# Optimization experiments

Hardware: AMD Instinct MI355X
Metric: run time of the kernel (lower is better)

The kernel has to match this reference:

```python
import jax, jax.numpy as jnp
import numpy as np
from jax import lax

NUM_CLASSES = 10
NUM_ITER = 3
CAP_DIM = 8       # primary capsule dim
OUT_CAP_DIM = 16  # digit capsule dim
NUM_MAP = 32      # 256 / 8
NUM_PRIM = 144    # 12*12


def squash(x, axis=-1):
    s2 = jnp.sum(x * x, axis=axis, keepdims=True)
    return (s2 / (1.0 + s2)) * x / jnp.sqrt(s2 + 1e-8)


def conv2d(x, w, b):
    y = lax.conv_general_dilated(x, w, (1, 1), 'VALID',
                                 dimension_numbers=('NCHW', 'OIHW', 'NCHW'))
    return y + b[None, :, None, None]


def setup_inputs() -> dict:
    key = jax.random.key(0)
    ks = jax.random.split(key, 13)
    B = 128
    return {
        'imgs': jax.random.uniform(ks[0], (B, 1, 28, 28), dtype=jnp.float32),
        'conv1_w': jax.random.normal(ks[1], (256, 1, 9, 9), jnp.float32) * 0.05,
        'conv1_b': jnp.zeros((256,), jnp.float32),
        'conv2_w': jax.random.normal(ks[2], (256, 256, 9, 9), jnp.float32) * 0.02,
        'conv2_b': jnp.zeros((256,), jnp.float32),
        # non-shared routing weights: [num_prim_map, num_prim_cap, num_classes, out_dim, in_dim]
        'W_digit': jax.random.normal(ks[3], (NUM_MAP, NUM_PRIM, NUM_CLASSES, OUT_CAP_DIM, CAP_DIM), jnp.float32),
        'dec_w1': jax.random.normal(ks[4], (OUT_CAP_DIM * NUM_CLASSES, 512), jnp.float32) * 0.05,
        'dec_b1': jnp.zeros((512,), jnp.float32),
        'dec_w2': jax.random.normal(ks[5], (512, 1024), jnp.float32) * 0.04,
        'dec_b2': jnp.zeros((1024,), jnp.float32),
        'dec_w3': jax.random.normal(ks[6], (1024, 784), jnp.float32) * 0.03,
        'dec_b3': jnp.zeros((784,), jnp.float32),
    }


def capsnet_fwd(imgs, conv1_w, conv1_b, conv2_w, conv2_b, W_digit,
                dec_w1, dec_b1, dec_w2, dec_b2, dec_w3, dec_b3):
    B = imgs.shape[0]
    # conv1 + relu: [B,256,20,20]
    x = jax.nn.relu(conv2d(imgs, conv1_w, conv1_b))
    # primary caps conv: [B,256,12,12]
    p = conv2d(x, conv2_w, conv2_b)
    # view [B, cap_dim, num_map, 12, 12] -> [B, num_map, 144, cap_dim]
    p = p.reshape(B, CAP_DIM, NUM_MAP, NUM_PRIM)
    p = jnp.transpose(p, (0, 2, 3, 1))
    u = squash(p, axis=-1)  # [B, 32, 144, 8]

    # u_hat[b,m,p,c,o] = W[m,p,c,o,i] * u[b,m,p,i]  (broadcast instead of repeat)
    u_hat = jnp.einsum('mpcoi,bmpi->bmpco', W_digit, u)
    u_hat = u_hat.reshape(B, NUM_MAP * NUM_PRIM, NUM_CLASSES, OUT_CAP_DIM)  # [B,4608,10,16]

    # dynamic routing
    b_ij = jnp.zeros((B, NUM_MAP * NUM_PRIM, NUM_CLASSES), u_hat.dtype)
    v = None
    for i in range(NUM_ITER):
        c_ij = jax.nn.softmax(b_ij, axis=1)                     # over input capsules
        s_j = jnp.einsum('bnc,bncd->bcd', c_ij, u_hat)          # [B,10,16]
        v = squash(s_j, axis=-1)
        if i != NUM_ITER - 1:
            b_ij = b_ij + jnp.einsum('bncd,bcd->bnc', u_hat, v)  # agreement

    # v: [B,10,16]
    v_length = jnp.sqrt(jnp.sum(v * v, axis=-1))                 # [B,10]
    y_pred = jnp.argmax(v_length, axis=1)
    y_pred_ohe = jax.nn.one_hot(y_pred, NUM_CLASSES, dtype=jnp.int32)

    masked = (v * y_pred_ohe.astype(v.dtype)[:, :, None]).reshape(B, -1)  # [B,160]
    h = jax.nn.relu(masked @ dec_w1 + dec_b1)
    h = jax.nn.relu(h @ dec_w2 + dec_b2)
    img_reconst = jax.nn.sigmoid(h @ dec_w3 + dec_b3)            # [B,784]
    return y_pred_ohe, img_reconst, v_length


def reference(imgs, conv1_w, conv1_b, conv2_w, conv2_b, W_digit,
              dec_w1, dec_b1, dec_w2, dec_b2, dec_w3, dec_b3):
    return capsnet_fwd(imgs, conv1_w, conv1_b, conv2_w, conv2_b, W_digit,
                       dec_w1, dec_b1, dec_w2, dec_b2, dec_w3, dec_b3)
```

## Files before the change

### kernel.cpp

```cpp
#include <hip/hip_runtime.h>
#include <cstdint>
#include <cstddef>

#define BB 128
#define NMAP 32
#define NPRIM 144
#define NCAP 4608
#define NCLS 10
#define ODIM 16
#define IDIM 8

#define WS_X1H  0
#define WS_X1L  6553600
#define WS_BH   13107200
#define WS_BL   15761408
#define WS_P    18415616
#define WS_U    23134208
#define WS_V    27852800
#define WS_H1   27873280
#define WS_H2   27938816
#define WS_CLS  28069888

#define OUT_REC  1280
#define OUT_LEN  101632

typedef __attribute__((ext_vector_type(8))) short short8;
typedef __attribute__((ext_vector_type(4))) float f32x4;

static __device__ __forceinline__ ushort f2bf(float f) {
    uint u = __float_as_uint(f);
    u = (u + 0x7FFFu + ((u >> 16) & 1u)) >> 16;
    return (ushort)u;
}
static __device__ __forceinline__ float bf2f(ushort h) {
    return __uint_as_float(((uint)h) << 16);
}


__global__ __launch_bounds__(256) void k_conv1(const float* __restrict__ img,
                                               const float* __restrict__ w,
                                               const float* __restrict__ bias,
                                               ushort* __restrict__ x1h,
                                               ushort* __restrict__ x1l) {
    __shared__ float simg[252];
    int bi = blockIdx.x;
    int y = bi % 20;
    int b = bi / 20;
    int oc = threadIdx.x;
    if (threadIdx.x < 252)
        simg[threadIdx.x] = img[(size_t)b * 784 + y * 28 + threadIdx.x];
    __syncthreads();

    float acc[20];
    float bv = bias[oc];
#pragma unroll
    for (int x = 0; x < 20; ++x) acc[x] = bv;
    const float* wp = w + oc * 81;
#pragma unroll
    for (int kh = 0; kh < 9; ++kh) {
        float r[28];
#pragma unroll
        for (int j = 0; j < 28; ++j) r[j] = simg[kh * 28 + j];
#pragma unroll
        for (int kw = 0; kw < 9; ++kw) {
            float wv = wp[kh * 9 + kw];
#pragma unroll
            for (int x = 0; x < 20; ++x)
                acc[x] = fmaf(wv, r[x + kw], acc[x]);
        }
    }
    size_t base = ((size_t)b * 400 + y * 20) * 256 + oc;
#pragma unroll
    for (int x = 0; x < 20; ++x) {
        float v = fmaxf(acc[x], 0.f);
        ushort h = f2bf(v);
        ushort lo = f2bf(v - bf2f(h));
        x1h[base + (size_t)x * 256] = h;
        x1l[base + (size_t)x * 256] = lo;
    }
}

__global__ __launch_bounds__(256) void k_prep_w(const float* __restrict__ w2,
                                                ushort* __restrict__ bh,
                                                ushort* __restrict__ bl) {
    int id = blockIdx.x * 256 + threadIdx.x;
    const float* src = w2 + (size_t)id * 81;
#pragma unroll 9
    for (int t = 0; t < 81; ++t) {
        float v = src[t];
        ushort h = f2bf(v);
        ushort lo = f2bf(v - bf2f(h));
        bh[(size_t)t * 65536 + id] = h;
        bl[(size_t)t * 65536 + id] = lo;
    }
}

static __device__ __forceinline__ f32x4 mfma16(short8 a, short8 b, f32x4 c) {
    return __builtin_amdgcn_mfma_f32_16x16x32_bf16(a, b, c, 0, 0, 0);
}

template<int NMF>
static __device__ __forceinline__ void tap_loop(
    f32x4 (&acc)[5][2], const ushort* A_lds, const int* celloff,
    const ushort* __restrict__ wbh, const ushort* __restrict__ wbl,
    int boff0, int boff1, int bicc) {
    short8 ah[2][5], al[2][5], bhr[2][2], blr[2][2];
#pragma unroll
    for (int i = 0; i < NMF; ++i) {
        ah[0][i] = *(const short8*)(A_lds + celloff[i]);
        al[0][i] = *(const short8*)(A_lds + 16000 + celloff[i]);
    }
    bhr[0][0] = *(const short8*)(wbh + bicc + boff0);
    bhr[0][1] = *(const short8*)(wbh + bicc + boff1);
    blr[0][0] = *(const short8*)(wbl + bicc + boff0);
    blr[0][1] = *(const short8*)(wbl + bicc + boff1);

#pragma unroll 2
    for (int t = 0; t < 81; ++t) {
        const int cur = t & 1, nxt = cur ^ 1;
        if (t < 80) {
            int tn = t + 1;
            int kh = tn / 9, kw = tn - kh * 9;
            int tapoff = (kh * 20 + kw) * 40;
            size_t bko = (size_t)tn * 65536 + bicc;
            bhr[nxt][0] = *(const short8*)(wbh + bko + boff0);
            bhr[nxt][1] = *(const short8*)(wbh + bko + boff1);
            blr[nxt][0] = *(const short8*)(wbl + bko + boff0);
            blr[nxt][1] = *(const short8*)(wbl + bko + boff1);
#pragma unroll
            for (int i = 0; i < NMF; ++i) {
                ah[nxt][i] = *(const short8*)(A_lds + tapoff + celloff[i]);
                al[nxt][i] = *(const short8*)(A_lds + 16000 + tapoff + celloff[i]);
            }
        }
#pragma unroll
        for (int i = 0; i < NMF; ++i)
#pragma unroll
            for (int j = 0; j < 2; ++j)
                acc[i][j] = mfma16(ah[cur][i], bhr[cur][j], acc[i][j]);
#pragma unroll
        for (int i = 0; i < NMF; ++i)
#pragma unroll
            for (int j = 0; j < 2; ++j)
                acc[i][j] = mfma16(ah[cur][i], blr[cur][j], acc[i][j]);
#pragma unroll
        for (int i = 0; i < NMF; ++i)
#pragma unroll
            for (int j = 0; j < 2; ++j)
                acc[i][j] = mfma16(al[cur][i], bhr[cur][j], acc[i][j]);
    }
}

template<int MF0, int NMF>
static __device__ __forceinline__ void conv2s_epi(
    const f32x4 (&acc)[5][2], const float* __restrict__ bias,
    float* __restrict__ p, int b, int oc0, int nq, int r, int kq) {
#pragma unroll
    for (int j = 0; j < 2; ++j) {
        int oc = oc0 + (nq * 2 + j) * 16 + r;
        float bv = bias[oc];
#pragma unroll
        for (int i = 0; i < NMF; ++i) {
            int row = b * 144 + (MF0 + i) * 16 + kq * 4;
#pragma unroll
            for (int reg = 0; reg < 4; ++reg)
                p[(size_t)(row + reg) * 256 + oc] = acc[i][j][reg] + bv;
        }
    }
}

__global__ __launch_bounds__(512, 2) void k_conv2s(
    const ushort* __restrict__ x1h, const ushort* __restrict__ x1l,
    const ushort* __restrict__ wbh, const ushort* __restrict__ wbl,
    const float* __restrict__ bias, float* __restrict__ p) {
    __shared__ ushort A_lds[32000];

    const int tid = threadIdx.x;
    const int lane = tid & 63;
    const int wv = tid >> 6;
    const int mh = wv >> 2;
    const int nq = wv & 3;
    const int b  = blockIdx.x >> 1;
    const int nt = blockIdx.x & 1;
    const int oc0 = nt * 128;
    const int r = lane & 15, kq = lane >> 4;
    const int MF0r = mh ? 5 : 0;

    int celloff[5];
#pragma unroll
    for (int i = 0; i < 5; ++i) {
        int lm = (MF0r + i) * 16 + r;
        celloff[i] = ((lm / 12) * 20 + (lm % 12)) * 40 + kq * 8;
    }
    const int boff0 = (oc0 + (nq * 2 + 0) * 16 + r) * 256 + kq * 8;
    const int boff1 = (oc0 + (nq * 2 + 1) * 16 + r) * 256 + kq * 8;

    f32x4 acc[5][2];
#pragma unroll
    for (int i = 0; i < 5; ++i)
#pragma unroll
        for (int j = 0; j < 2; ++j)
            acc[i][j] = (f32x4){0.f, 0.f, 0.f, 0.f};

    for (int icc = 0; icc < 8; ++icc) {
        if (icc) __syncthreads();
#pragma unroll
        for (int rd = 0; rd < 7; ++rd) {
            int idx = rd * 512 + tid;
            if (idx < 3200) {
                int comp = (idx >= 1600) ? 1 : 0;
                int ci = idx - comp * 1600;
                int cell = ci >> 2, cc = ci & 3;
                const ushort* src = (comp ? x1l : x1h) +
                    ((size_t)b * 400 + cell) * 256 + icc * 32 + cc * 8;
                short8 val = *(const short8*)src;
                *(short8*)(A_lds + comp * 16000 + cell * 40 + cc * 8) = val;
            }
        }
        __syncthreads();
        int bicc = icc * 32;
        if (mh == 0) tap_loop<5>(acc, A_lds, celloff, wbh, wbl, boff0, boff1, bicc);
        else         tap_loop<4>(acc, A_lds, celloff, wbh, wbl, boff0, boff1, bicc);
    }

    if (mh == 0) conv2s_epi<0, 5>(acc, bias, p, b, oc0, nq, r, kq);
    else         conv2s_epi<5, 4>(acc, bias, p, b, oc0, nq, r, kq);
}

__global__ __launch_bounds__(256) void k_squash(const float* __restrict__ p,
                                                float* __restrict__ u) {
    int id = blockIdx.x * 256 + threadIdx.x;
    int n = id % NCAP;
    int b = id / NCAP;
    int m = n / NPRIM, pos = n - m * NPRIM;
    const float* pp = p + ((size_t)b * 144 + pos) * 256 + m;
    float pv[8];
    float s2 = 0.f;
#pragma unroll
    for (int i = 0; i < 8; ++i) {
        pv[i] = pp[i * 32];
        s2 = fmaf(pv[i], pv[i], s2);
    }
    float f = (s2 / (1.f + s2)) / sqrtf(s2 + 1e-8f);
    float4 a = make_float4(f * pv[0], f * pv[1], f * pv[2], f * pv[3]);
    float4 c = make_float4(f * pv[4], f * pv[5], f * pv[6], f * pv[7]);
    float4* up = (float4*)(u + (size_t)id * 8);
    up[0] = a;
    up[1] = c;
}

__global__ __launch_bounds__(256) void k_prep_wt(const float* __restrict__ Wd,
                                                 float* __restrict__ Wt) {
    __shared__ float S[64][129];
    int c = blockIdx.x % NCLS;
    int nt = blockIdx.x / NCLS;
    int n0 = nt * 64;
    int tid = threadIdx.x;
#pragma unroll
    for (int rep = 0; rep < 32; ++rep) {
        int idx = rep * 256 + tid;
        int nl = idx >> 7, oi = idx & 127;
        S[nl][oi] = Wd[(size_t)(n0 + nl) * 1280 + c * 128 + oi];
    }
    __syncthreads();
#pragma unroll
    for (int rep = 0; rep < 32; ++rep) {
        int idx = rep * 256 + tid;
        int oi = idx >> 6, nl = idx & 63;
        Wt[((size_t)c * 128 + oi) * NCAP + n0 + nl] = S[nl][oi];
    }
}

__global__ __launch_bounds__(256) void k_route5(const float* __restrict__ u,
                                                const float* __restrict__ Wt,
                                                float* __restrict__ v_out) {
    __shared__ float part[4][2][17];
    __shared__ float sums[2][17];
    __shared__ float vsh[2][16];
    int c = blockIdx.x % NCLS;
    int bg = blockIdx.x / NCLS;
    int b0 = bg * 2;
    int tid = threadIdx.x;
    int lane = tid & 63, wvi = tid >> 6;
    const float* WtC = Wt + (size_t)c * 128 * NCAP;

    float bij[18][2];
#pragma unroll
    for (int j = 0; j < 18; ++j) { bij[j][0] = 0.f; bij[j][1] = 0.f; }

    for (int iter = 0; iter < 3; ++iter) {
        float sZ[2] = {0.f, 0.f};
        float sS[2][16];
#pragma unroll
        for (int o = 0; o < 16; ++o) { sS[0][o] = 0.f; sS[1][o] = 0.f; }

        for (int j = 0; j < 18; ++j) {
            int n = j * 256 + tid;
            const float4* up0 = (const float4*)(u + ((size_t)b0 * NCAP + n) * 8);
            const float4* up1 = (const float4*)(u + ((size_t)(b0 + 1) * NCAP + n) * 8);
            float4 a0 = up0[0], a1 = up0[1];
            float4 c0 = up1[0], c1 = up1[1];
            float u0[8] = {a0.x, a0.y, a0.z, a0.w, a1.x, a1.y, a1.z, a1.w};
            float u1[8] = {c0.x, c0.y, c0.z, c0.w, c1.x, c1.y, c1.z, c1.w};
            float uh[2][16];
#pragma unroll
            for (int o = 0; o < 16; ++o) {
                float s0 = 0.f, s1 = 0.f;
#pragma unroll
                for (int i = 0; i < 8; ++i) {
                    float w = WtC[(size_t)(o * 8 + i) * NCAP + n];
                    s0 = fmaf(w, u0[i], s0);
                    s1 = fmaf(w, u1[i], s1);
                }
                uh[0][o] = s0;
                uh[1][o] = s1;
            }
#pragma unroll
            for (int bb = 0; bb < 2; ++bb) {
                float e;
                if (iter == 0) {
                    e = 1.f;
                } else {
                    float agr = 0.f;
#pragma unroll
                    for (int o = 0; o < 16; ++o) agr = fmaf(uh[bb][o], vsh[bb][o], agr);
                    bij[j][bb] += agr;
                    e = __expf(bij[j][bb]);
                }
                sZ[bb] += e;
#pragma unroll
                for (int o = 0; o < 16; ++o) sS[bb][o] = fmaf(e, uh[bb][o], sS[bb][o]);
            }
        }

#pragma unroll
        for (int bb = 0; bb < 2; ++bb) {
            float z = sZ[bb];
#pragma unroll
            for (int d = 32; d >= 1; d >>= 1) z += __shfl_xor(z, d, 64);
            if (lane == 0) part[wvi][bb][0] = z;
#pragma unroll
            for (int o = 0; o < 16; ++o) {
                float s = sS[bb][o];
#pragma unroll
                for (int d = 32; d >= 1; d >>= 1) s += __shfl_xor(s, d, 64);
                if (lane == 0) part[wvi][bb][1 + o] = s;
            }
        }
        __syncthreads();
        if (tid < 34) {
            int bb = tid / 17, k = tid % 17;
            float s = 0.f;
#pragma unroll
            for (int w4 = 0; w4 < 4; ++w4) s += part[w4][bb][k];
            sums[bb][k] = s;
        }
        __syncthreads();
        if (tid < 2) {
            float Z = sums[tid][0];
            float s[16];
            float s2 = 0.f;
#pragma unroll
            for (int o = 0; o < 16; ++o) {
                s[o] = sums[tid][1 + o] / Z;
                s2 = fmaf(s[o], s[o], s2);
            }
            float f = (s2 / (1.f + s2)) / sqrtf(s2 + 1e-8f);
#pragma unroll
            for (int o = 0; o < 16; ++o) vsh[tid][o] = f * s[o];
        }
        __syncthreads();
    }
    if (tid < 32) {
        int bb = tid >> 4, o = tid & 15;
        v_out[((size_t)(b0 + bb) * NCLS + c) * 16 + o] = vsh[bb][o];
    }
}

__global__ __launch_bounds__(64) void k_head(const float* __restrict__ v,
                                             float* __restrict__ out,
                                             int* __restrict__ cls_ws) {
    __shared__ float len2[NCLS];
    __shared__ int cls_sh;
    int b = blockIdx.x, tid = threadIdx.x;
    if (tid < NCLS) {
        float s2 = 0.f;
#pragma unroll
        for (int o = 0; o < 16; ++o) {
            float t = v[((size_t)b * NCLS + tid) * 16 + o];
            s2 = fmaf(t, t, s2);
        }
        len2[tid] = s2;
        out[OUT_LEN + b * NCLS + tid] = sqrtf(s2);
    }
    __syncthreads();
    if (tid == 0) {
        int best = 0;
        float bv = len2[0];
        for (int c2 = 1; c2 < NCLS; ++c2)
            if (len2[c2] > bv) { bv = len2[c2]; best = c2; }
        cls_sh = best;
        cls_ws[b] = best;
    }
    __syncthreads();
    if (tid < NCLS) out[b * NCLS + tid] = (tid == cls_sh) ? 1.0f : 0.0f;
}

__global__ __launch_bounds__(256) void k_dec1(const float* __restrict__ v,
                                              const int* __restrict__ cls_ws,
                                              const float* __restrict__ w1,
                                              const float* __restrict__ b1,
                                              float* __restrict__ h1) {
    int id = blockIdx.x * 256 + threadIdx.x;
    int j = id % 512, b = id / 512;
    int cls = cls_ws[b];
    const float* vp = v + ((size_t)b * NCLS + cls) * 16;
    float acc = b1[j];
#pragma unroll
    for (int o = 0; o < 16; ++o)
        acc = fmaf(vp[o], w1[(size_t)(cls * 16 + o) * 512 + j], acc);
    h1[id] = fmaxf(acc, 0.f);
}

__global__ __launch_bounds__(256) void k_dec2(const float* __restrict__ h1,
                                              const float* __restrict__ w2,
                                              const float* __restrict__ b2,
                                              float* __restrict__ h2) {
    __shared__ float hs[512];
    int bi = blockIdx.x;
    int jc = bi % 4;
    int b = bi / 4;
    int tid = threadIdx.x;
    hs[tid] = h1[b * 512 + tid];
    hs[tid + 256] = h1[b * 512 + tid + 256];
    __syncthreads();
    int j = jc * 256 + tid;
    float acc = b2[j];
#pragma unroll 8
    for (int k = 0; k < 512; ++k)
        acc = fmaf(hs[k], w2[(size_t)k * 1024 + j], acc);
    h2[b * 1024 + j] = fmaxf(acc, 0.f);
}

__global__ __launch_bounds__(256) void k_dec3(const float* __restrict__ h2,
                                              const float* __restrict__ w3,
                                              const float* __restrict__ b3,
                                              float* __restrict__ out) {
    __shared__ float hs[1024];
    int bi = blockIdx.x;
    int jc = bi % 4;
    int b = bi / 4;
    int tid = threadIdx.x;
#pragma unroll
    for (int t = 0; t < 4; ++t) hs[tid + t * 256] = h2[b * 1024 + tid + t * 256];
    __syncthreads();
    int j = jc * 256 + tid;
    if (j < 784) {
        float acc = b3[j];
#pragma unroll 8
        for (int k = 0; k < 1024; ++k)
            acc = fmaf(hs[k], w3[(size_t)k * 784 + j], acc);
        out[OUT_REC + b * 784 + j] = 1.f / (1.f + __expf(-acc));
    }
}

extern "C" void kernel_launch(void* const* d_in, const int* in_sizes, int n_in,
                              void* d_out, int out_size, void* d_ws, size_t ws_size,
                              hipStream_t stream) {
    const float* imgs = (const float*)d_in[0];
    const float* c1w  = (const float*)d_in[1];
    const float* c1b  = (const float*)d_in[2];
    const float* c2w  = (const float*)d_in[3];
    const float* c2b  = (const float*)d_in[4];
    const float* Wd   = (const float*)d_in[5];
    const float* dw1  = (const float*)d_in[6];
    const float* db1  = (const float*)d_in[7];
    const float* dw2  = (const float*)d_in[8];
    const float* db2  = (const float*)d_in[9];
    const float* dw3  = (const float*)d_in[10];
    const float* db3  = (const float*)d_in[11];

    float* out = (float*)d_out;
    float* ws  = (float*)d_ws;
    ushort* x1h = (ushort*)(ws + WS_X1H);
    ushort* x1l = (ushort*)(ws + WS_X1L);
    ushort* wbh = (ushort*)(ws + WS_BH);
    ushort* wbl = (ushort*)(ws + WS_BL);
    float* p    = ws + WS_P;
    float* u    = ws + WS_U;
    float* v    = ws + WS_V;
    float* h1   = ws + WS_H1;
    float* h2   = ws + WS_H2;
    int*   cls  = (int*)(ws + WS_CLS);
    float* wt32 = ws + WS_X1H;

    k_conv1<<<BB * 20, 256, 0, stream>>>(imgs, c1w, c1b, x1h, x1l);
    k_prep_w<<<256, 256, 0, stream>>>(c2w, wbh, wbl);
    k_conv2s<<<BB * 2, 512, 0, stream>>>(x1h, x1l, wbh, wbl, c2b, p);
    k_squash<<<BB * NCAP / 256, 256, 0, stream>>>(p, u);
    k_prep_wt<<<720, 256, 0, stream>>>(Wd, wt32);
    k_route5<<<(BB / 2) * NCLS, 256, 0, stream>>>(u, wt32, v);
    k_head<<<BB, 64, 0, stream>>>(v, out, cls);
    k_dec1<<<BB * 512 / 256, 256, 0, stream>>>(v, cls, dw1, db1, h1);
    k_dec2<<<BB * 4, 256, 0, stream>>>(h1, dw2, db2, h2);
    k_dec3<<<BB * 4, 256, 0, stream>>>(h2, dw3, db3, out);
}
```

Baseline: 1.304 ms.

## Retile conv2 MFMA waves to 3x4 fragments with ping-pong fragment buffers

Changes the per-wave tile in the primary-caps conv from 5x2 to 3x4 MFMA fragments, splitting M across four wave groups and N across two. The tap loop becomes an explicit two-buffer ping-pong with separate load and compute helpers. This raises MFMA count per loaded fragment and reduces LDS reads of A. The costs are more global weight fragment loads per wave and an imbalanced split in which the first wave group does 3 M tiles while the others do 2.

New measurement: 1.851 ms. +42.0%, slower.

```diff
diff --git a/kernel.cpp b/kernel.cpp
--- a/kernel.cpp
+++ b/kernel.cpp
@@ -99,69 +99,78 @@
     return __builtin_amdgcn_mfma_f32_16x16x32_bf16(a, b, c, 0, 0, 0);
 }
 
+
+template<int NMF>
+static __device__ __forceinline__ void load_frags(
+    short8 (&ah)[3], short8 (&al)[3], short8 (&bh)[4], short8 (&bl)[4],
+    const ushort* A_lds, const int* celloff,
+    const ushort* __restrict__ wbh, const ushort* __restrict__ wbl,
+    const int* boff, int tn, int bicc) {
+    int kh = tn / 9, kw = tn - kh * 9;
+    int tapoff = (kh * 20 + kw) * 40;
+    size_t bko = (size_t)tn * 65536 + bicc;
+#pragma unroll
+    for (int i = 0; i < NMF; ++i) {
+        ah[i] = *(const short8*)(A_lds + tapoff + celloff[i]);
+        al[i] = *(const short8*)(A_lds + 16000 + tapoff + celloff[i]);
+    }
+#pragma unroll
+    for (int j = 0; j < 4; ++j) {
+        bh[j] = *(const short8*)(wbh + bko + boff[j]);
+        bl[j] = *(const short8*)(wbl + bko + boff[j]);
+    }
+}
+
+template<int NMF>
+static __device__ __forceinline__ void compute_frags(
+    f32x4 (&acc)[3][4], const short8 (&ah)[3], const short8 (&al)[3],
+    const short8 (&bh)[4], const short8 (&bl)[4]) {
+#pragma unroll
+    for (int i = 0; i < NMF; ++i)
+#pragma unroll
+        for (int j = 0; j < 4; ++j)
+            acc[i][j] = mfma16(ah[i], bh[j], acc[i][j]);
+#pragma unroll
+    for (int i = 0; i < NMF; ++i)
+#pragma unroll
+        for (int j = 0; j < 4; ++j)
+            acc[i][j] = mfma16(ah[i], bl[j], acc[i][j]);
+#pragma unroll
+    for (int i = 0; i < NMF; ++i)
+#pragma unroll
+        for (int j = 0; j < 4; ++j)
+            acc[i][j] = mfma16(al[i], bh[j], acc[i][j]);
+}
+
 template<int NMF>
 static __device__ __forceinline__ void tap_loop(
-    f32x4 (&acc)[5][2], const ushort* A_lds, const int* celloff,
+    f32x4 (&acc)[3][4], const ushort* A_lds, const int* celloff,
     const ushort* __restrict__ wbh, const ushort* __restrict__ wbl,
-    int boff0, int boff1, int bicc) {
-    short8 ah[2][5], al[2][5], bhr[2][2], blr[2][2];
-#pragma unroll
-    for (int i = 0; i < NMF; ++i) {
-        ah[0][i] = *(const short8*)(A_lds + celloff[i]);
-        al[0][i] = *(const short8*)(A_lds + 16000 + celloff[i]);
-    }
-    bhr[0][0] = *(const short8*)(wbh + bicc + boff0);
-    bhr[0][1] = *(const short8*)(wbh + bicc + boff1);
-    blr[0][0] = *(const short8*)(wbl + bicc + boff0);
-    blr[0][1] = *(const short8*)(wbl + bicc + boff1);
-
-#pragma unroll 2
-    for (int t = 0; t < 81; ++t) {
-        const int cur = t & 1, nxt = cur ^ 1;
-        if (t < 80) {
-            int tn = t + 1;
-            int kh = tn / 9, kw = tn - kh * 9;
-            int tapoff = (kh * 20 + kw) * 40;
-            size_t bko = (size_t)tn * 65536 + bicc;
-            bhr[nxt][0] = *(const short8*)(wbh + bko + boff0);
-            bhr[nxt][1] = *(const short8*)(wbh + bko + boff1);
-            blr[nxt][0] = *(const short8*)(wbl + bko + boff0);
-            blr[nxt][1] = *(const short8*)(wbl + bko + boff1);
-#pragma unroll
-            for (int i = 0; i < NMF; ++i) {
-                ah[nxt][i] = *(const short8*)(A_lds + tapoff + celloff[i]);
-                al[nxt][i] = *(const short8*)(A_lds + 16000 + tapoff + celloff[i]);
-            }
-        }
-#pragma unroll
-        for (int i = 0; i < NMF; ++i)
-#pragma unroll
-            for (int j = 0; j < 2; ++j)
-                acc[i][j] = mfma16(ah[cur][i], bhr[cur][j], acc[i][j]);
-#pragma unroll
-        for (int i = 0; i < NMF; ++i)
-#pragma unroll
-            for (int j = 0; j < 2; ++j)
-                acc[i][j] = mfma16(ah[cur][i], blr[cur][j], acc[i][j]);
-#pragma unroll
-        for (int i = 0; i < NMF; ++i)
-#pragma unroll
-            for (int j = 0; j < 2; ++j)
-                acc[i][j] = mfma16(al[cur][i], bhr[cur][j], acc[i][j]);
-    }
-}
-
-template<int MF0, int NMF>
+    const int* boff, int bicc) {
+    short8 ah0[3], al0[3], bh0[4], bl0[4];
+    short8 ah1[3], al1[3], bh1[4], bl1[4];
+    load_frags<NMF>(ah0, al0, bh0, bl0, A_lds, celloff, wbh, wbl, boff, 0, bicc);
+#pragma unroll 1
+    for (int t = 0; t < 80; t += 2) {
+        load_frags<NMF>(ah1, al1, bh1, bl1, A_lds, celloff, wbh, wbl, boff, t + 1, bicc);
+        compute_frags<NMF>(acc, ah0, al0, bh0, bl0);
+        load_frags<NMF>(ah0, al0, bh0, bl0, A_lds, celloff, wbh, wbl, boff, t + 2, bicc);
+        compute_frags<NMF>(acc, ah1, al1, bh1, bl1);
+    }
+    compute_frags<NMF>(acc, ah0, al0, bh0, bl0);
+}
+
+template<int NMF>
 static __device__ __forceinline__ void conv2s_epi(
-    const f32x4 (&acc)[5][2], const float* __restrict__ bias,
-    float* __restrict__ p, int b, int oc0, int nq, int r, int kq) {
-#pragma unroll
-    for (int j = 0; j < 2; ++j) {
-        int oc = oc0 + (nq * 2 + j) * 16 + r;
+    const f32x4 (&acc)[3][4], const float* __restrict__ bias,
+    float* __restrict__ p, int b, int oc0, int mt0, int nq, int r, int kq) {
+#pragma unroll
+    for (int j = 0; j < 4; ++j) {
+        int oc = oc0 + (nq * 4 + j) * 16 + r;
         float bv = bias[oc];
 #pragma unroll
         for (int i = 0; i < NMF; ++i) {
-            int row = b * 144 + (MF0 + i) * 16 + kq * 4;
+            int row = b * 144 + (mt0 + i) * 16 + kq * 4;
 #pragma unroll
             for (int reg = 0; reg < 4; ++reg)
                 p[(size_t)(row + reg) * 256 + oc] = acc[i][j][reg] + bv;
@@ -178,28 +187,30 @@
     const int tid = threadIdx.x;
     const int lane = tid & 63;
     const int wv = tid >> 6;
-    const int mh = wv >> 2;
-    const int nq = wv & 3;
+    const int mh = wv >> 1;
+    const int nq = wv & 1;
     const int b  = blockIdx.x >> 1;
     const int nt = blockIdx.x & 1;
     const int oc0 = nt * 128;
     const int r = lane & 15, kq = lane >> 4;
-    const int MF0r = mh ? 5 : 0;
-
-    int celloff[5];
-#pragma unroll
-    for (int i = 0; i < 5; ++i) {
-        int lm = (MF0r + i) * 16 + r;
+    const int mt0 = mh ? (2 * mh + 1) : 0;
+
+    int celloff[3];
+#pragma unroll
+    for (int i = 0; i < 3; ++i) {
+        int lm = (mt0 + i) * 16 + r;
         celloff[i] = ((lm / 12) * 20 + (lm % 12)) * 40 + kq * 8;
     }
-    const int boff0 = (oc0 + (nq * 2 + 0) * 16 + r) * 256 + kq * 8;
-    const int boff1 = (oc0 + (nq * 2 + 1) * 16 + r) * 256 + kq * 8;
-
-    f32x4 acc[5][2];
-#pragma unroll
-    for (int i = 0; i < 5; ++i)
-#pragma unroll
-        for (int j = 0; j < 2; ++j)
+    int boff[4];
+#pragma unroll
+    for (int j = 0; j < 4; ++j)
+        boff[j] = (oc0 + (nq * 4 + j) * 16 + r) * 256 + kq * 8;
+
+    f32x4 acc[3][4];
+#pragma unroll
+    for (int i = 0; i < 3; ++i)
+#pragma unroll
+        for (int j = 0; j < 4; ++j)
             acc[i][j] = (f32x4){0.f, 0.f, 0.f, 0.f};
 
     for (int icc = 0; icc < 8; ++icc) {
@@ -219,12 +230,12 @@
         }
         __syncthreads();
         int bicc = icc * 32;
-        if (mh == 0) tap_loop<5>(acc, A_lds, celloff, wbh, wbl, boff0, boff1, bicc);
-        else         tap_loop<4>(acc, A_lds, celloff, wbh, wbl, boff0, boff1, bicc);
-    }
-
-    if (mh == 0) conv2s_epi<0, 5>(acc, bias, p, b, oc0, nq, r, kq);
-    else         conv2s_epi<5, 4>(acc, bias, p, b, oc0, nq, r, kq);
+        if (mh == 0) tap_loop<3>(acc, A_lds, celloff, wbh, wbl, boff, bicc);
+        else         tap_loop<2>(acc, A_lds, celloff, wbh, wbl, boff, bicc);
+    }
+
+    if (mh == 0) conv2s_epi<3>(acc, bias, p, b, oc0, mt0, nq, r, kq);
+    else         conv2s_epi<2>(acc, bias, p, b, oc0, mt0, nq, r, kq);
 }
 
 __global__ __launch_bounds__(256) void k_squash(const float* __restrict__ p,
```

## Stage conv2 weight tiles into LDS with async global-to-LDS double buffering

Applied to the files above, without the earlier changes.

The bf16 hi/lo conv2 weights are repacked into one per-tap, per-channel-chunk layout. Each tap's tile is then copied into a double-buffered LDS region with global_load_lds, instead of every wave loading its B fragments straight from global memory. This removes duplicate global weight reads across the M-half waves and lets the next tap's copy overlap the current tap's MFMAs. The cost is a block-wide barrier after every tap and a larger LDS footprint, which could limit occupancy and adds synchronisation overhead.

Result: no change. 1.299 ms (-0.4%).

```diff
diff --git a/kernel.cpp b/kernel.cpp
--- a/kernel.cpp
+++ b/kernel.cpp
@@ -13,7 +13,6 @@
 #define WS_X1H  0
 #define WS_X1L  6553600
 #define WS_BH   13107200
-#define WS_BL   15761408
 #define WS_P    18415616
 #define WS_U    23134208
 #define WS_V    27852800
@@ -34,6 +33,12 @@
 }
 static __device__ __forceinline__ float bf2f(ushort h) {
     return __uint_as_float(((uint)h) << 16);
+}
+
+static __device__ __forceinline__ void gload16(const ushort* g, ushort* l) {
+    __builtin_amdgcn_global_load_lds(
+        (const __attribute__((address_space(1))) void*)g,
+        (__attribute__((address_space(3))) void*)l, 16, 0, 0);
 }
 
 
@@ -80,18 +85,23 @@
     }
 }
 
-__global__ __launch_bounds__(256) void k_prep_w(const float* __restrict__ w2,
-                                                ushort* __restrict__ bh,
-                                                ushort* __restrict__ bl) {
-    int id = blockIdx.x * 256 + threadIdx.x;
-    const float* src = w2 + (size_t)id * 81;
+__global__ __launch_bounds__(256) void k_prep_w2(const float* __restrict__ w2,
+                                                 ushort* __restrict__ bpk) {
+    int blk = blockIdx.x;
+    int icc = blk >> 5, kq = (blk >> 3) & 3, ocg = blk & 7;
+    int tid = threadIdx.x;
+    int ocl = tid >> 3, ic8 = tid & 7;
+    int oc = ocg * 32 + ocl;
+    int ic = icc * 32 + kq * 8 + ic8;
+    const float* src = w2 + ((size_t)oc * 256 + ic) * 81;
+    size_t dbase = (size_t)icc * 16384 + (size_t)kq * 2048 + (size_t)oc * 8 + ic8;
 #pragma unroll 9
     for (int t = 0; t < 81; ++t) {
         float v = src[t];
         ushort h = f2bf(v);
         ushort lo = f2bf(v - bf2f(h));
-        bh[(size_t)t * 65536 + id] = h;
-        bl[(size_t)t * 65536 + id] = lo;
+        bpk[(size_t)t * 131072 + dbase] = h;
+        bpk[(size_t)t * 131072 + dbase + 8192] = lo;
     }
 }
 
@@ -99,55 +109,35 @@
     return __builtin_amdgcn_mfma_f32_16x16x32_bf16(a, b, c, 0, 0, 0);
 }
 
+
 template<int NMF>
-static __device__ __forceinline__ void tap_loop(
-    f32x4 (&acc)[5][2], const ushort* A_lds, const int* celloff,
-    const ushort* __restrict__ wbh, const ushort* __restrict__ wbl,
-    int boff0, int boff1, int bicc) {
-    short8 ah[2][5], al[2][5], bhr[2][2], blr[2][2];
+static __device__ __forceinline__ void tap_body(
+    f32x4 (&acc)[5][2], const ushort* A_lds, const ushort* Bc,
+    const int* celloff, int tapoff, int bro0, int bro1) {
+    short8 ah[5], al[5];
 #pragma unroll
     for (int i = 0; i < NMF; ++i) {
-        ah[0][i] = *(const short8*)(A_lds + celloff[i]);
-        al[0][i] = *(const short8*)(A_lds + 16000 + celloff[i]);
-    }
-    bhr[0][0] = *(const short8*)(wbh + bicc + boff0);
-    bhr[0][1] = *(const short8*)(wbh + bicc + boff1);
-    blr[0][0] = *(const short8*)(wbl + bicc + boff0);
-    blr[0][1] = *(const short8*)(wbl + bicc + boff1);
-
-#pragma unroll 2
-    for (int t = 0; t < 81; ++t) {
-        const int cur = t & 1, nxt = cur ^ 1;
-        if (t < 80) {
-            int tn = t + 1;
-            int kh = tn / 9, kw = tn - kh * 9;
-            int tapoff = (kh * 20 + kw) * 40;
-            size_t bko = (size_t)tn * 65536 + bicc;
-            bhr[nxt][0] = *(const short8*)(wbh + bko + boff0);
-            bhr[nxt][1] = *(const short8*)(wbh + bko + boff1);
-            blr[nxt][0] = *(const short8*)(wbl + bko + boff0);
-            blr[nxt][1] = *(const short8*)(wbl + bko + boff1);
-#pragma unroll
-            for (int i = 0; i < NMF; ++i) {
-                ah[nxt][i] = *(const short8*)(A_lds + tapoff + celloff[i]);
-                al[nxt][i] = *(const short8*)(A_lds + 16000 + tapoff + celloff[i]);
-            }
-        }
-#pragma unroll
-        for (int i = 0; i < NMF; ++i)
-#pragma unroll
-            for (int j = 0; j < 2; ++j)
-                acc[i][j] = mfma16(ah[cur][i], bhr[cur][j], acc[i][j]);
-#pragma unroll
-        for (int i = 0; i < NMF; ++i)
-#pragma unroll
-            for (int j = 0; j < 2; ++j)
-                acc[i][j] = mfma16(ah[cur][i], blr[cur][j], acc[i][j]);
-#pragma unroll
-        for (int i = 0; i < NMF; ++i)
-#pragma unroll
-            for (int j = 0; j < 2; ++j)
-                acc[i][j] = mfma16(al[cur][i], bhr[cur][j], acc[i][j]);
+        ah[i] = *(const short8*)(A_lds + tapoff + celloff[i]);
+        al[i] = *(const short8*)(A_lds + 16000 + tapoff + celloff[i]);
+    }
+    short8 bh0 = *(const short8*)(Bc + bro0);
+    short8 bh1 = *(const short8*)(Bc + bro1);
+    short8 bl0 = *(const short8*)(Bc + 4096 + bro0);
+    short8 bl1 = *(const short8*)(Bc + 4096 + bro1);
+#pragma unroll
+    for (int i = 0; i < NMF; ++i) {
+        acc[i][0] = mfma16(ah[i], bh0, acc[i][0]);
+        acc[i][1] = mfma16(ah[i], bh1, acc[i][1]);
+    }
+#pragma unroll
+    for (int i = 0; i < NMF; ++i) {
+        acc[i][0] = mfma16(ah[i], bl0, acc[i][0]);
+        acc[i][1] = mfma16(ah[i], bl1, acc[i][1]);
+    }
+#pragma unroll
+    for (int i = 0; i < NMF; ++i) {
+        acc[i][0] = mfma16(al[i], bh0, acc[i][0]);
+        acc[i][1] = mfma16(al[i], bh1, acc[i][1]);
     }
 }
 
@@ -171,9 +161,10 @@
 
 __global__ __launch_bounds__(512, 2) void k_conv2s(
     const ushort* __restrict__ x1h, const ushort* __restrict__ x1l,
-    const ushort* __restrict__ wbh, const ushort* __restrict__ wbl,
+    const ushort* __restrict__ bpk,
     const float* __restrict__ bias, float* __restrict__ p) {
-    __shared__ ushort A_lds[32000];
+    __shared__ __align__(16) ushort A_lds[32000];
+    __shared__ __align__(16) ushort Bb[16384];
 
     const int tid = threadIdx.x;
     const int lane = tid & 63;
@@ -192,8 +183,12 @@
         int lm = (MF0r + i) * 16 + r;
         celloff[i] = ((lm / 12) * 20 + (lm % 12)) * 40 + kq * 8;
     }
-    const int boff0 = (oc0 + (nq * 2 + 0) * 16 + r) * 256 + kq * 8;
-    const int boff1 = (oc0 + (nq * 2 + 1) * 16 + r) * 256 + kq * 8;
+    const int bro0 = kq * 1024 + ((nq * 2 + 0) * 16 + r) * 8;
+    const int bro1 = kq * 1024 + ((nq * 2 + 1) * 16 + r) * 8;
+
+    const int comp_w = wv >> 2, kq_w = wv & 3;
+    const ushort* gB0 = bpk + comp_w * 8192 + kq_w * 2048 + oc0 * 8 + lane * 8;
+    ushort* lB0 = Bb + comp_w * 4096 + kq_w * 1024;
 
     f32x4 acc[5][2];
 #pragma unroll
@@ -203,7 +198,6 @@
             acc[i][j] = (f32x4){0.f, 0.f, 0.f, 0.f};
 
     for (int icc = 0; icc < 8; ++icc) {
-        if (icc) __syncthreads();
 #pragma unroll
         for (int rd = 0; rd < 7; ++rd) {
             int idx = rd * 512 + tid;
@@ -217,10 +211,28 @@
                 *(short8*)(A_lds + comp * 16000 + cell * 40 + cc * 8) = val;
             }
         }
+        {
+            size_t goff = (size_t)icc * 16384;
+            gload16(gB0 + goff, lB0);
+            gload16(gB0 + goff + 512, lB0 + 512);
+        }
         __syncthreads();
-        int bicc = icc * 32;
-        if (mh == 0) tap_loop<5>(acc, A_lds, celloff, wbh, wbl, boff0, boff1, bicc);
-        else         tap_loop<4>(acc, A_lds, celloff, wbh, wbl, boff0, boff1, bicc);
+
+#pragma unroll 2
+        for (int t = 0; t < 81; ++t) {
+            const int cur = t & 1;
+            if (t < 80) {
+                size_t goff = (size_t)(t + 1) * 131072 + (size_t)icc * 16384;
+                gload16(gB0 + goff, lB0 + (cur ^ 1) * 8192);
+                gload16(gB0 + goff + 512, lB0 + (cur ^ 1) * 8192 + 512);
+            }
+            int kh = t / 9, kw = t - kh * 9;
+            int tapoff = (kh * 20 + kw) * 40;
+            const ushort* Bc = Bb + cur * 8192;
+            if (mh == 0) tap_body<5>(acc, A_lds, Bc, celloff, tapoff, bro0, bro1);
+            else         tap_body<4>(acc, A_lds, Bc, celloff, tapoff, bro0, bro1);
+            __syncthreads();
+        }
     }
 
     if (mh == 0) conv2s_epi<0, 5>(acc, bias, p, b, oc0, nq, r, kq);
@@ -484,8 +496,7 @@
     float* ws  = (float*)d_ws;
     ushort* x1h = (ushort*)(ws + WS_X1H);
     ushort* x1l = (ushort*)(ws + WS_X1L);
-    ushort* wbh = (ushort*)(ws + WS_BH);
-    ushort* wbl = (ushort*)(ws + WS_BL);
+    ushort* bpk = (ushort*)(ws + WS_BH);
     float* p    = ws + WS_P;
     float* u    = ws + WS_U;
     float* v    = ws + WS_V;
@@ -495,8 +506,8 @@
     float* wt32 = ws + WS_X1H;
 
     k_conv1<<<BB * 20, 256, 0, stream>>>(imgs, c1w, c1b, x1h, x1l);
-    k_prep_w<<<256, 256, 0, stream>>>(c2w, wbh, wbl);
-    k_conv2s<<<BB * 2, 512, 0, stream>>>(x1h, x1l, wbh, wbl, c2b, p);
+    k_prep_w2<<<256, 256, 0, stream>>>(c2w, bpk);
+    k_conv2s<<<BB * 2, 512, 0, stream>>>(x1h, x1l, bpk, c2b, p);
     k_squash<<<BB * NCAP / 256, 256, 0, stream>>>(p, u);
     k_prep_wt<<<720, 256, 0, stream>>>(Wd, wt32);
     k_route5<<<(BB / 2) * NCLS, 256, 0, stream>>>(u, wt32, v);
```
